# Kernel optimization log

Hardware: AMD Instinct MI355X
Metric: run time of the kernel (lower is better)

The kernel has to match this reference:

```python
import jax, jax.numpy as jnp
import numpy as np
from jax import lax

IMAGE_SIZE = 1280
STRIDE = 32
FMP = IMAGE_SIZE // STRIDE          # 40
BPC = 5                             # boxes per cell (5 anchors)
NUM_CLASSES = 80
NMS_THRESH = 0.5
CONF_THRESH = 0.3
N_BOX = FMP * FMP * BPC             # 8000 candidates
ANCHOR_SIZE = np.array([[17, 25], [55, 75], [92, 206], [202, 21], [289, 311]], dtype=np.float32)


def _make_anchors():
    # generate_anchors: per-cell (x,y) grid repeated for each of BPC anchors, tiled anchor wh
    ys, xs = jnp.meshgrid(jnp.arange(FMP, dtype=jnp.float32), jnp.arange(FMP, dtype=jnp.float32), indexing='ij')
    xy = jnp.stack([xs, ys], axis=-1).reshape(-1, 1, 2)                       # [HW,1,2]
    anchor_xy = jnp.broadcast_to(xy, (FMP * FMP, BPC, 2)).reshape(-1, 2)      # [N,2]
    anchor_wh = jnp.broadcast_to(jnp.asarray(ANCHOR_SIZE)[None], (FMP * FMP, BPC, 2)).reshape(-1, 2)
    return jnp.concatenate([anchor_xy, anchor_wh], axis=-1)                   # [N,4]


def setup_inputs() -> dict:
    key = jax.random.key(0)
    k = jax.random.split(key, 5)
    return {
        'cls_feat': jax.random.normal(k[0], (1, 512, FMP, FMP), jnp.float32),
        'reg_feat': jax.random.normal(k[1], (1, 512, FMP, FMP), jnp.float32),
        'w_obj': jax.random.normal(k[2], (BPC, 512), jnp.float32) * 0.02,
        'b_obj': jnp.zeros((BPC,), jnp.float32),
        'w_cls': jax.random.normal(k[3], (NUM_CLASSES * BPC, 512), jnp.float32) * 0.02,
        'b_cls': jnp.zeros((NUM_CLASSES * BPC,), jnp.float32),
        'w_reg': jax.random.normal(k[4], (4 * BPC, 512), jnp.float32) * 0.02,
        'b_reg': jnp.zeros((4 * BPC,), jnp.float32),
    }


def reference(cls_feat, reg_feat, w_obj, b_obj, w_cls, b_cls, w_reg, b_reg):
    # 1x1 convs as channel contractions, already permuted to NHWC like permute(0,2,3,1)
    obj = (jnp.einsum('bchw,oc->bhwo', reg_feat, w_obj) + b_obj).reshape(-1, 1)            # [N,1]
    cls = (jnp.einsum('bchw,oc->bhwo', cls_feat, w_cls) + b_cls).reshape(-1, NUM_CLASSES)  # [N,C]
    reg = (jnp.einsum('bchw,oc->bhwo', reg_feat, w_reg) + b_reg).reshape(-1, 4)            # [N,4]

    scores = jnp.sqrt(jax.nn.sigmoid(obj) * jax.nn.sigmoid(cls))                           # [N,C]

    # decode_boxes
    anchors = _make_anchors()
    ctr = (jax.nn.sigmoid(reg[:, :2]) + anchors[:, :2]) * STRIDE
    wh = jnp.exp(reg[:, 2:]) * anchors[:, 2:]
    bboxes = jnp.concatenate([ctr - wh * 0.5, ctr + wh * 0.5], axis=-1)                    # [N,4] x1y1x2y2

    # postprocess: per-box best class + confidence filter
    labels = jnp.argmax(scores, axis=1)
    score = jnp.take_along_axis(scores, labels[:, None], axis=1)[:, 0]
    valid = score >= CONF_THRESH

    # faithful to original nms(): it re-interprets decoded x1y1x2y2 as cxcywh before IoU
    b2 = jnp.concatenate([bboxes[:, :2] - bboxes[:, 2:] * 0.5,
                          bboxes[:, :2] + bboxes[:, 2:] * 0.5], axis=-1)

    # greedy per-class NMS == global greedy with cross-class IoU gated to 0
    order = jnp.argsort(-score)
    bs = b2[order]
    ls = labels[order]
    vs = valid[order]
    areas = (bs[:, 2] - bs[:, 0]) * (bs[:, 3] - bs[:, 1])
    xx1 = jnp.maximum(bs[:, None, 0], bs[None, :, 0])
    yy1 = jnp.maximum(bs[:, None, 1], bs[None, :, 1])
    xx2 = jnp.minimum(bs[:, None, 2], bs[None, :, 2])
    yy2 = jnp.minimum(bs[:, None, 3], bs[None, :, 3])
    inter = jnp.maximum(1e-10, xx2 - xx1) * jnp.maximum(1e-10, yy2 - yy1)
    iou = inter / (areas[:, None] + areas[None, :] - inter + 1e-14)                        # [N,N]
    same = ls[:, None] == ls[None, :]

    idx = jnp.arange(N_BOX)

    def body(k, supp):
        active = vs[k] & jnp.logical_not(supp[k])
        row = active & (iou[k] > NMS_THRESH) & same[k] & (idx > k)
        return supp | row

    supp = lax.fori_loop(0, N_BOX, body, jnp.zeros(N_BOX, bool))
    keep = jnp.zeros(N_BOX, bool).at[order].set(vs & jnp.logical_not(supp))

    # fixed-size masked outputs (original returns variable-length filtered arrays)
    return bboxes, score, labels, keep
```

## Files before the change

kernel.cpp:

```cpp
#include <hip/hip_runtime.h>
#include <math.h>

#define FMPX 40
#define NPOS 1600
#define NCLS 80
#define NBOX 8000
#define KDIM 512
#define KC   64
#define CAP  256

__constant__ float c_aw[5] = {17.f, 55.f, 92.f, 202.f, 289.f};
__constant__ float c_ah[5] = {25.f, 75.f, 206.f, 21.f, 311.f};

__device__ __forceinline__ float sigf(float x) { return 1.0f / (1.0f + expf(-x)); }

__global__ __launch_bounds__(256) void k_gemm(
    const float* __restrict__ cls_feat, const float* __restrict__ reg_feat,
    const float* __restrict__ w_obj, const float* __restrict__ b_obj,
    const float* __restrict__ w_cls, const float* __restrict__ b_cls,
    const float* __restrict__ w_reg, const float* __restrict__ b_reg,
    float* __restrict__ clsRaw,
    float* __restrict__ roRaw)
{
    __shared__ float Ws[16 * KDIM];
    __shared__ float As[KC * 64];
    const int mTile = blockIdx.x;
    const int nTile = blockIdx.y;
    const int hw0   = mTile * 64;
    const bool isCls = (nTile < 25);
    const float* feat = isCls ? cls_feat : reg_feat;

    const int pos = threadIdx.x & 63;
    const int og  = threadIdx.x >> 6;

    for (int i = threadIdx.x * 4; i < 16 * KDIM; i += 256 * 4) {
        int r = i >> 9, k = i & 511;
        const float* src;
        bool valid = true;
        if (isCls) {
            src = w_cls + (nTile * 16 + r) * KDIM + k;
        } else {
            int o = (nTile - 25) * 16 + r;
            if (o < 5)       src = w_obj + o * KDIM + k;
            else if (o < 25) src = w_reg + (o - 5) * KDIM + k;
            else           { src = w_obj; valid = false; }
        }
        float4 v = valid ? *(const float4*)src : make_float4(0.f, 0.f, 0.f, 0.f);
        *(float4*)&Ws[i] = v;
    }

    float bias[4];
    bool ok[4];
#pragma unroll
    for (int j = 0; j < 4; j++) {
        int r = og * 4 + j;
        if (isCls) {
            bias[j] = b_cls[nTile * 16 + r]; ok[j] = true;
        } else {
            int o = (nTile - 25) * 16 + r;
            if (o < 5)       { bias[j] = b_obj[o];     ok[j] = true; }
            else if (o < 25) { bias[j] = b_reg[o - 5]; ok[j] = true; }
            else             { bias[j] = 0.0f;         ok[j] = false; }
        }
    }

    float acc[4] = {0.f, 0.f, 0.f, 0.f};
    const float* wsBase = &Ws[(og * 4) * KDIM];

    for (int kc = 0; kc < KDIM; kc += KC) {
        for (int i = threadIdx.x * 4; i < KC * 64; i += 256 * 4) {
            int r = i >> 6, c = i & 63;
            *(float4*)&As[i] = *(const float4*)&feat[(kc + r) * NPOS + hw0 + c];
        }
        __syncthreads();

        for (int kk = 0; kk < KC; kk += 8) {
            float a[8];
#pragma unroll
            for (int t = 0; t < 8; t++) a[t] = As[(kk + t) * 64 + pos];
#pragma unroll
            for (int j = 0; j < 4; j++) {
                const float* wp = wsBase + j * KDIM + kc + kk;
                float4 wA = *(const float4*)wp;
                float4 wB = *(const float4*)(wp + 4);
                acc[j] += a[0] * wA.x; acc[j] += a[1] * wA.y;
                acc[j] += a[2] * wA.z; acc[j] += a[3] * wA.w;
                acc[j] += a[4] * wB.x; acc[j] += a[5] * wB.y;
                acc[j] += a[6] * wB.z; acc[j] += a[7] * wB.w;
            }
        }
        __syncthreads();
    }

    const int hw = hw0 + pos;
    if (isCls) {
        float4 rv = make_float4(acc[0] + bias[0], acc[1] + bias[1],
                                acc[2] + bias[2], acc[3] + bias[3]);
        *(float4*)&clsRaw[hw * 400 + nTile * 16 + og * 4] = rv;
    } else {
#pragma unroll
        for (int j = 0; j < 4; j++) {
            int o = (nTile - 25) * 16 + og * 4 + j;
            if (ok[j]) roRaw[hw * 25 + o] = acc[j] + bias[j];
        }
    }
}

__global__ __launch_bounds__(256) void k_box(
    const float* __restrict__ clsRaw, const float* __restrict__ roRaw,
    float* __restrict__ out,
    float4* __restrict__ nmsBox, float* __restrict__ nmsArea,
    float* __restrict__ listScore, int* __restrict__ listIdx, int* __restrict__ counts)
{
    const int n = blockIdx.x * 4 + (threadIdx.x >> 6);
    const int lane = threadIdx.x & 63;
    const int hw = n / 5, a = n % 5;

    const float sobj = sigf(roRaw[hw * 25 + a]);
    const float* cbase = clsRaw + hw * 400 + a * 80;

    float v = sqrtf(sobj * sigf(cbase[lane]));
    int bi = lane;
    if (lane < 16) {
        float s2 = sqrtf(sobj * sigf(cbase[64 + lane]));
        if (s2 > v) { v = s2; bi = 64 + lane; }
    }
#pragma unroll
    for (int off = 32; off >= 1; off >>= 1) {
        float ov = __shfl_xor(v, off);
        int   oi = __shfl_xor(bi, off);
        if (ov > v || (ov == v && oi < bi)) { v = ov; bi = oi; }
    }

    if (lane == 0) {
        const float* rp = roRaw + hw * 25 + 5 + a * 4;
        float r0 = rp[0], r1 = rp[1], r2 = rp[2], r3 = rp[3];
        float gx = (float)(hw % FMPX), gy = (float)(hw / FMPX);
        float cx = (sigf(r0) + gx) * 32.0f;
        float cy = (sigf(r1) + gy) * 32.0f;
        float wv = expf(r2) * c_aw[a];
        float hv = expf(r3) * c_ah[a];
        float x1 = cx - wv * 0.5f, y1 = cy - hv * 0.5f;
        float x2 = cx + wv * 0.5f, y2 = cy + hv * 0.5f;

        out[n * 4 + 0] = x1; out[n * 4 + 1] = y1;
        out[n * 4 + 2] = x2; out[n * 4 + 3] = y2;
        out[32000 + n] = v;
        out[40000 + n] = (float)bi;
        out[48000 + n] = 0.0f;

        float nx1 = x1 - x2 * 0.5f, ny1 = y1 - y2 * 0.5f;
        float nx2 = x1 + x2 * 0.5f, ny2 = y1 + y2 * 0.5f;
        nmsBox[n]  = make_float4(nx1, ny1, nx2, ny2);
        nmsArea[n] = (nx2 - nx1) * (ny2 - ny1);

        if (v >= 0.3f) {
            int p = atomicAdd(&counts[bi], 1);
            if (p < CAP) { listScore[bi * CAP + p] = v; listIdx[bi * CAP + p] = n; }
        }
    }
}

__global__ __launch_bounds__(64) void k_nms(
    const float* __restrict__ listScore, const int* __restrict__ listIdx,
    const int* __restrict__ counts,
    const float4* __restrict__ nmsBox, const float* __restrict__ nmsArea,
    float* __restrict__ keepOut)
{
    const int c = blockIdx.x;
    int m = counts[c];
    if (m > CAP) m = CAP;

    int P = 2;
    while (P < m) P <<= 1;

    __shared__ float ss[CAP];
    __shared__ int   si[CAP];
    __shared__ float bx1[CAP], by1[CAP], bx2[CAP], by2[CAP], bar[CAP];
    __shared__ int   supp[CAP];

    for (int i = threadIdx.x; i < P; i += 64) {
        if (i < m) { ss[i] = listScore[c * CAP + i]; si[i] = listIdx[c * CAP + i]; }
        else       { ss[i] = -INFINITY;              si[i] = 0x7FFFFFFF; }
    }
    __syncthreads();

    for (int size = 2; size <= P; size <<= 1) {
        for (int stride = size >> 1; stride > 0; stride >>= 1) {
            for (int t = threadIdx.x; t < P / 2; t += 64) {
                int lo = 2 * stride * (t / stride) + (t % stride);
                int hi = lo + stride;
                bool desc = ((lo & size) == 0);
                float slo = ss[lo], shi = ss[hi];
                int   ilo = si[lo], ihi = si[hi];
                bool loBetter = (slo > shi) || (slo == shi && ilo < ihi);
                bool doSwap = desc ? !loBetter : loBetter;
                if (doSwap) { ss[lo] = shi; ss[hi] = slo; si[lo] = ihi; si[hi] = ilo; }
            }
            __syncthreads();
        }
    }

    for (int i = threadIdx.x; i < m; i += 64) {
        int n = si[i];
        float4 b = nmsBox[n];
        bx1[i] = b.x; by1[i] = b.y; bx2[i] = b.z; by2[i] = b.w;
        bar[i] = nmsArea[n];
        supp[i] = 0;
    }
    __syncthreads();

    for (int k = 0; k < m; k++) {
        if (!supp[k]) {
            float kx1 = bx1[k], ky1 = by1[k], kx2 = bx2[k], ky2 = by2[k], ka = bar[k];
            for (int j = k + 1 + threadIdx.x; j < m; j += 64) {
                float xx1 = fmaxf(kx1, bx1[j]);
                float yy1 = fmaxf(ky1, by1[j]);
                float xx2 = fminf(kx2, bx2[j]);
                float yy2 = fminf(ky2, by2[j]);
                float inter = fmaxf(1e-10f, xx2 - xx1) * fmaxf(1e-10f, yy2 - yy1);
                float iou = inter / ((ka + bar[j] - inter) + 1e-14f);
                if (iou > 0.5f) supp[j] = 1;
            }
        }
        __syncthreads();
    }

    for (int j = threadIdx.x; j < m; j += 64) {
        if (!supp[j]) keepOut[si[j]] = 1.0f;
    }
}

extern "C" void kernel_launch(void* const* d_in, const int* in_sizes, int n_in,
                              void* d_out, int out_size, void* d_ws, size_t ws_size,
                              hipStream_t stream) {
    const float* cls_feat = (const float*)d_in[0];
    const float* reg_feat = (const float*)d_in[1];
    const float* w_obj    = (const float*)d_in[2];
    const float* b_obj    = (const float*)d_in[3];
    const float* w_cls    = (const float*)d_in[4];
    const float* b_cls    = (const float*)d_in[5];
    const float* w_reg    = (const float*)d_in[6];
    const float* b_reg    = (const float*)d_in[7];

    float* out = (float*)d_out;
    float* ws  = (float*)d_ws;

    float*  clsRaw    = ws;
    float*  roRaw     = ws + 640000;
    float4* nmsBox    = (float4*)(ws + 680000);
    float*  nmsArea   = ws + 712000;
    float*  listScore = ws + 720000;
    int*    listIdx   = (int*)(ws + 740480);
    int*    counts    = (int*)(ws + 760960);

    hipMemsetAsync(counts, 0, NCLS * sizeof(int), stream);

    k_gemm<<<dim3(25, 27), 256, 0, stream>>>(cls_feat, reg_feat,
                                             w_obj, b_obj, w_cls, b_cls, w_reg, b_reg,
                                             clsRaw, roRaw);
    k_box<<<NBOX / 4, 256, 0, stream>>>(clsRaw, roRaw, out, nmsBox, nmsArea,
                                        listScore, listIdx, counts);
    k_nms<<<NCLS, 64, 0, stream>>>(listScore, listIdx, counts, nmsBox, nmsArea,
                                   out + 48000);
}
```

Baseline: 184.8 us.

## Register-prefetch GEMM activations, vectorize class argmax, build NMS lists in-kernel

The GEMM drops the shared-memory activation tile and its per-chunk barriers. Each thread instead streams its own activation column from global memory into double-buffered registers, overlapping the next loads with the current FMAs. The box kernel reads class logits as float4, four per lane, and no longer does global atomics. The NMS kernel now scans all 8000 score/label pairs per class, gathers them with shared-memory atomics, runs with 256 threads, and removes the memset. The trade-off is that every NMS block rescans the full candidate array, and global activation loads go uncached through LDS.

After: 149.5 us. 1.24x faster.

```diff
diff --git a/kernel.cpp b/kernel.cpp
--- a/kernel.cpp
+++ b/kernel.cpp
@@ -6,7 +6,6 @@
 #define NCLS 80
 #define NBOX 8000
 #define KDIM 512
-#define KC   64
 #define CAP  256
 
 __constant__ float c_aw[5] = {17.f, 55.f, 92.f, 202.f, 289.f};
@@ -23,7 +22,6 @@
     float* __restrict__ roRaw)
 {
     __shared__ float Ws[16 * KDIM];
-    __shared__ float As[KC * 64];
     const int mTile = blockIdx.x;
     const int nTile = blockIdx.y;
     const int hw0   = mTile * 64;
@@ -32,6 +30,14 @@
 
     const int pos = threadIdx.x & 63;
     const int og  = threadIdx.x >> 6;
+
+    const float* ap = feat + hw0 + pos;
+
+    float A0[8], A1[8];
+#pragma unroll
+    for (int t = 0; t < 8; t++) A0[t] = ap[t * NPOS];
+#pragma unroll
+    for (int t = 0; t < 8; t++) A1[t] = ap[(8 + t) * NPOS];
 
     for (int i = threadIdx.x * 4; i < 16 * KDIM; i += 256 * 4) {
         int r = i >> 9, k = i & 511;
@@ -64,32 +70,51 @@
         }
     }
 
+    __syncthreads();
+
     float acc[4] = {0.f, 0.f, 0.f, 0.f};
     const float* wsBase = &Ws[(og * 4) * KDIM];
 
-    for (int kc = 0; kc < KDIM; kc += KC) {
-        for (int i = threadIdx.x * 4; i < KC * 64; i += 256 * 4) {
-            int r = i >> 6, c = i & 63;
-            *(float4*)&As[i] = *(const float4*)&feat[(kc + r) * NPOS + hw0 + c];
-        }
-        __syncthreads();
-
-        for (int kk = 0; kk < KC; kk += 8) {
-            float a[8];
-#pragma unroll
-            for (int t = 0; t < 8; t++) a[t] = As[(kk + t) * 64 + pos];
-#pragma unroll
-            for (int j = 0; j < 4; j++) {
-                const float* wp = wsBase + j * KDIM + kc + kk;
-                float4 wA = *(const float4*)wp;
-                float4 wB = *(const float4*)(wp + 4);
-                acc[j] += a[0] * wA.x; acc[j] += a[1] * wA.y;
-                acc[j] += a[2] * wA.z; acc[j] += a[3] * wA.w;
-                acc[j] += a[4] * wB.x; acc[j] += a[5] * wB.y;
-                acc[j] += a[6] * wB.z; acc[j] += a[7] * wB.w;
-            }
-        }
-        __syncthreads();
+    for (int kk = 0; kk < KDIM - 16; kk += 16) {
+#pragma unroll
+        for (int j = 0; j < 4; j++) {
+            const float* wp = wsBase + j * KDIM + kk;
+            acc[j] += A0[0] * wp[0]; acc[j] += A0[1] * wp[1];
+            acc[j] += A0[2] * wp[2]; acc[j] += A0[3] * wp[3];
+            acc[j] += A0[4] * wp[4]; acc[j] += A0[5] * wp[5];
+            acc[j] += A0[6] * wp[6]; acc[j] += A0[7] * wp[7];
+        }
+#pragma unroll
+        for (int t = 0; t < 8; t++) A0[t] = ap[(kk + 16 + t) * NPOS];
+#pragma unroll
+        for (int j = 0; j < 4; j++) {
+            const float* wp = wsBase + j * KDIM + kk + 8;
+            acc[j] += A1[0] * wp[0]; acc[j] += A1[1] * wp[1];
+            acc[j] += A1[2] * wp[2]; acc[j] += A1[3] * wp[3];
+            acc[j] += A1[4] * wp[4]; acc[j] += A1[5] * wp[5];
+            acc[j] += A1[6] * wp[6]; acc[j] += A1[7] * wp[7];
+        }
+#pragma unroll
+        for (int t = 0; t < 8; t++) A1[t] = ap[(kk + 24 + t) * NPOS];
+    }
+    {
+        const int kk = KDIM - 16;
+#pragma unroll
+        for (int j = 0; j < 4; j++) {
+            const float* wp = wsBase + j * KDIM + kk;
+            acc[j] += A0[0] * wp[0]; acc[j] += A0[1] * wp[1];
+            acc[j] += A0[2] * wp[2]; acc[j] += A0[3] * wp[3];
+            acc[j] += A0[4] * wp[4]; acc[j] += A0[5] * wp[5];
+            acc[j] += A0[6] * wp[6]; acc[j] += A0[7] * wp[7];
+        }
+#pragma unroll
+        for (int j = 0; j < 4; j++) {
+            const float* wp = wsBase + j * KDIM + kk + 8;
+            acc[j] += A1[0] * wp[0]; acc[j] += A1[1] * wp[1];
+            acc[j] += A1[2] * wp[2]; acc[j] += A1[3] * wp[3];
+            acc[j] += A1[4] * wp[4]; acc[j] += A1[5] * wp[5];
+            acc[j] += A1[6] * wp[6]; acc[j] += A1[7] * wp[7];
+        }
     }
 
     const int hw = hw0 + pos;
@@ -110,7 +135,7 @@
     const float* __restrict__ clsRaw, const float* __restrict__ roRaw,
     float* __restrict__ out,
     float4* __restrict__ nmsBox, float* __restrict__ nmsArea,
-    float* __restrict__ listScore, int* __restrict__ listIdx, int* __restrict__ counts)
+    float2* __restrict__ sl)
 {
     const int n = blockIdx.x * 4 + (threadIdx.x >> 6);
     const int lane = threadIdx.x & 63;
@@ -119,12 +144,19 @@
     const float sobj = sigf(roRaw[hw * 25 + a]);
     const float* cbase = clsRaw + hw * 400 + a * 80;
 
-    float v = sqrtf(sobj * sigf(cbase[lane]));
-    int bi = lane;
-    if (lane < 16) {
-        float s2 = sqrtf(sobj * sigf(cbase[64 + lane]));
-        if (s2 > v) { v = s2; bi = 64 + lane; }
-    }
+    const int l4 = (lane < 20) ? lane : 19;
+    float4 cs = *(const float4*)(cbase + l4 * 4);
+
+    float s0 = sqrtf(sobj * sigf(cs.x));
+    float s1 = sqrtf(sobj * sigf(cs.y));
+    float s2 = sqrtf(sobj * sigf(cs.z));
+    float s3 = sqrtf(sobj * sigf(cs.w));
+    float v = s0; int bi = l4 * 4;
+    if (s1 > v) { v = s1; bi = l4 * 4 + 1; }
+    if (s2 > v) { v = s2; bi = l4 * 4 + 2; }
+    if (s3 > v) { v = s3; bi = l4 * 4 + 3; }
+    if (lane >= 20) { v = -1.0f; bi = 0x7FFFFFFF; }
+
 #pragma unroll
     for (int off = 32; off >= 1; off >>= 1) {
         float ov = __shfl_xor(v, off);
@@ -148,46 +180,53 @@
         out[32000 + n] = v;
         out[40000 + n] = (float)bi;
         out[48000 + n] = 0.0f;
+        sl[n] = make_float2(v, (float)bi);
 
         float nx1 = x1 - x2 * 0.5f, ny1 = y1 - y2 * 0.5f;
         float nx2 = x1 + x2 * 0.5f, ny2 = y1 + y2 * 0.5f;
         nmsBox[n]  = make_float4(nx1, ny1, nx2, ny2);
         nmsArea[n] = (nx2 - nx1) * (ny2 - ny1);
-
-        if (v >= 0.3f) {
-            int p = atomicAdd(&counts[bi], 1);
-            if (p < CAP) { listScore[bi * CAP + p] = v; listIdx[bi * CAP + p] = n; }
-        }
-    }
-}
-
-__global__ __launch_bounds__(64) void k_nms(
-    const float* __restrict__ listScore, const int* __restrict__ listIdx,
-    const int* __restrict__ counts,
+    }
+}
+
+__global__ __launch_bounds__(256) void k_nms(
+    const float2* __restrict__ sl,
     const float4* __restrict__ nmsBox, const float* __restrict__ nmsArea,
     float* __restrict__ keepOut)
 {
     const int c = blockIdx.x;
-    int m = counts[c];
-    if (m > CAP) m = CAP;
-
-    int P = 2;
-    while (P < m) P <<= 1;
 
     __shared__ float ss[CAP];
     __shared__ int   si[CAP];
     __shared__ float bx1[CAP], by1[CAP], bx2[CAP], by2[CAP], bar[CAP];
     __shared__ int   supp[CAP];
-
-    for (int i = threadIdx.x; i < P; i += 64) {
-        if (i < m) { ss[i] = listScore[c * CAP + i]; si[i] = listIdx[c * CAP + i]; }
-        else       { ss[i] = -INFINITY;              si[i] = 0x7FFFFFFF; }
+    __shared__ int   cnt;
+
+    if (threadIdx.x == 0) cnt = 0;
+    __syncthreads();
+
+    for (int i = threadIdx.x; i < NBOX; i += 256) {
+        float2 p = sl[i];
+        if (p.x >= 0.3f && (int)p.y == c) {
+            int q = atomicAdd(&cnt, 1);
+            if (q < CAP) { ss[q] = p.x; si[q] = i; }
+        }
+    }
+    __syncthreads();
+
+    int m = cnt;
+    if (m > CAP) m = CAP;
+
+    int P = 2;
+    while (P < m) P <<= 1;
+    for (int i = threadIdx.x; i < P; i += 256) {
+        if (i >= m) { ss[i] = -INFINITY; si[i] = 0x7FFFFFFF; }
     }
     __syncthreads();
 
     for (int size = 2; size <= P; size <<= 1) {
         for (int stride = size >> 1; stride > 0; stride >>= 1) {
-            for (int t = threadIdx.x; t < P / 2; t += 64) {
+            for (int t = threadIdx.x; t < P / 2; t += 256) {
                 int lo = 2 * stride * (t / stride) + (t % stride);
                 int hi = lo + stride;
                 bool desc = ((lo & size) == 0);
@@ -201,7 +240,7 @@
         }
     }
 
-    for (int i = threadIdx.x; i < m; i += 64) {
+    for (int i = threadIdx.x; i < m; i += 256) {
         int n = si[i];
         float4 b = nmsBox[n];
         bx1[i] = b.x; by1[i] = b.y; bx2[i] = b.z; by2[i] = b.w;
@@ -213,7 +252,7 @@
     for (int k = 0; k < m; k++) {
         if (!supp[k]) {
             float kx1 = bx1[k], ky1 = by1[k], kx2 = bx2[k], ky2 = by2[k], ka = bar[k];
-            for (int j = k + 1 + threadIdx.x; j < m; j += 64) {
+            for (int j = k + 1 + threadIdx.x; j < m; j += 256) {
                 float xx1 = fmaxf(kx1, bx1[j]);
                 float yy1 = fmaxf(ky1, by1[j]);
                 float xx2 = fminf(kx2, bx2[j]);
@@ -226,7 +265,7 @@
         __syncthreads();
     }
 
-    for (int j = threadIdx.x; j < m; j += 64) {
+    for (int j = threadIdx.x; j < m; j += 256) {
         if (!supp[j]) keepOut[si[j]] = 1.0f;
     }
 }
@@ -250,17 +289,11 @@
     float*  roRaw     = ws + 640000;
     float4* nmsBox    = (float4*)(ws + 680000);
     float*  nmsArea   = ws + 712000;
-    float*  listScore = ws + 720000;
-    int*    listIdx   = (int*)(ws + 740480);
-    int*    counts    = (int*)(ws + 760960);
-
-    hipMemsetAsync(counts, 0, NCLS * sizeof(int), stream);
+    float2* sl        = (float2*)(ws + 720000);
 
     k_gemm<<<dim3(25, 27), 256, 0, stream>>>(cls_feat, reg_feat,
                                              w_obj, b_obj, w_cls, b_cls, w_reg, b_reg,
                                              clsRaw, roRaw);
-    k_box<<<NBOX / 4, 256, 0, stream>>>(clsRaw, roRaw, out, nmsBox, nmsArea,
-                                        listScore, listIdx, counts);
-    k_nms<<<NCLS, 64, 0, stream>>>(listScore, listIdx, counts, nmsBox, nmsArea,
-                                   out + 48000);
-}
+    k_box<<<NBOX / 4, 256, 0, stream>>>(clsRaw, roRaw, out, nmsBox, nmsArea, sl);
+    k_nms<<<NCLS, 256, 0, stream>>>(sl, nmsBox, nmsArea, out + 48000);
+}
```
